# Optimization experiments

Hardware: AMD Instinct MI355X
Metric: run time of the kernel (lower is better)

Reference implementation:

```python
import jax, jax.numpy as jnp
import numpy as np

N, E, D, H = 100000, 1000000, 64, 64  # nodes, edges, input_dim, output_dim
EPS = 1e-5


def _lin(k, fi, fo):
    return jax.random.normal(k, (fi, fo), jnp.float32) / np.sqrt(fi)


def setup_inputs() -> dict:
    key = jax.random.key(0)
    ks = jax.random.split(key, 8)
    x = jax.random.normal(ks[0], (N, D), jnp.float32)
    e = jax.random.uniform(ks[1], (E,), jnp.float32)
    edge_index = jax.random.randint(ks[2], (2, E), 0, N, dtype=jnp.int32)
    return {
        "x": x,
        "e": e,
        "edge_index": edge_index,
        "W1": _lin(ks[3], 2 * D, H), "b1": jnp.zeros((H,), jnp.float32),
        "g1": jnp.ones((H,), jnp.float32), "be1": jnp.zeros((H,), jnp.float32),
        "W2": _lin(ks[4], H, H), "b2": jnp.zeros((H,), jnp.float32),
        "g2": jnp.ones((H,), jnp.float32), "be2": jnp.zeros((H,), jnp.float32),
        "W3": _lin(ks[5], H, H), "b3": jnp.zeros((H,), jnp.float32),
    }


def _layer_norm(h, g, b):
    mu = jnp.mean(h, axis=-1, keepdims=True)
    var = jnp.mean(jnp.square(h - mu), axis=-1, keepdims=True)
    return (h - mu) * jax.lax.rsqrt(var + EPS) * g + b


def reference(x, e, edge_index, W1, b1, g1, be1, W2, b2, g2, be2, W3, b3):
    start, end = edge_index[0], edge_index[1]
    we = e[:, None]  # [E,1]
    # edge-weighted gather-multiply-scatter_add, both directions
    mi = jax.ops.segment_sum(we * x[start], end, num_segments=N) \
       + jax.ops.segment_sum(we * x[end], start, num_segments=N)  # [N,D]
    h = jnp.concatenate([mi, x], axis=1)  # [N,2D]
    h = jnp.tanh(_layer_norm(h @ W1 + b1, g1, be1))
    h = jnp.tanh(_layer_norm(h @ W2 + b2, g2, be2))
    return h @ W3 + b3  # [N,H]
```

## Files before the change

### kernel.cpp

```cpp
#include <hip/hip_runtime.h>

typedef unsigned int u32;

#define NMAX 100000
#define EMAX 1000000
#define CAP 96
#define NSHMAX 12500

__device__ __align__(16) float g_mi[NMAX * 64];
__device__ int g_deg[8 * NSHMAX];
__device__ __align__(16) u32 g_adj[(size_t)8 * NSHMAX * CAP];

__global__ __launch_bounds__(256) void zero_deg(int n) {
    int i = blockIdx.x * 256 + threadIdx.x;
    if (i < n) g_deg[i] = 0;
}

__global__ __launch_bounds__(256) void fill_sharded(
    const int* __restrict__ src, const int* __restrict__ dst,
    const float* __restrict__ ew, int E, int NSH, int nchunk)
{
    int group = blockIdx.x & 7;
    int chunk = blockIdx.x >> 3;
    int stride = nchunk * 256;
    for (int e = chunk * 256 + threadIdx.x; e < E; e += stride) {
        int s = src[e], t = dst[e];
        float w = ew[e];
        int w15 = (int)(w * 32768.f + 0.5f);
        if (w15 > 32767) w15 = 32767;
        if ((s & 7) == group) {
            int idx = group * NSH + (s >> 3);
            int p = atomicAdd(&g_deg[idx], 1);
            if (p < CAP) g_adj[(size_t)idx * CAP + p] = ((u32)t << 15) | (u32)w15;
        }
        if ((t & 7) == group) {
            int idx = group * NSH + (t >> 3);
            int q = atomicAdd(&g_deg[idx], 1);
            if (q < CAP) g_adj[(size_t)idx * CAP + q] = ((u32)s << 15) | (u32)w15;
        }
    }
}

__global__ __launch_bounds__(256) void gather(const float* __restrict__ x,
                                              int N, int NSH) {
    int wid = (blockIdx.x * 256 + threadIdx.x) >> 6;
    int lane = threadIdx.x & 63;
    if (wid >= N) return;
    int idx = (wid & 7) * NSH + (wid >> 3);
    int cnt = g_deg[idx];
    if (cnt > CAP) cnt = CAP;
    const u32* row = g_adj + (size_t)idx * CAP;
    float acc = 0.f;

    for (int b = 0; b < cnt; b += 64) {
        int m = cnt - b;
        if (m > 64) m = 64;
        u32 ent = (lane < m) ? row[b + lane] : 0u;
        int nbr = (int)(ent >> 15);
        float wv = (float)(ent & 0x7FFFu) * (1.f / 32768.f);

        int j = 0;
        for (; j + 4 <= m; j += 4) {
            int n0 = __shfl(nbr, j + 0);
            int n1 = __shfl(nbr, j + 1);
            int n2 = __shfl(nbr, j + 2);
            int n3 = __shfl(nbr, j + 3);
            float w0 = __shfl(wv, j + 0);
            float w1 = __shfl(wv, j + 1);
            float w2 = __shfl(wv, j + 2);
            float w3 = __shfl(wv, j + 3);
            float v0 = x[(size_t)n0 * 64 + lane];
            float v1 = x[(size_t)n1 * 64 + lane];
            float v2 = x[(size_t)n2 * 64 + lane];
            float v3 = x[(size_t)n3 * 64 + lane];
            acc = fmaf(w0, v0, acc);
            acc = fmaf(w1, v1, acc);
            acc = fmaf(w2, v2, acc);
            acc = fmaf(w3, v3, acc);
        }
        for (; j < m; j++) {
            int nb = __shfl(nbr, j);
            float w = __shfl(wv, j);
            acc = fmaf(w, x[(size_t)nb * 64 + lane], acc);
        }
    }
    g_mi[(size_t)wid * 64 + lane] = acc;
}

#define MST 65

__global__ __launch_bounds__(128) void mlp(
    const float* __restrict__ x,
    const float* __restrict__ W1, const float* __restrict__ B1,
    const float* __restrict__ G1, const float* __restrict__ E1,
    const float* __restrict__ W2, const float* __restrict__ B2,
    const float* __restrict__ G2, const float* __restrict__ E2,
    const float* __restrict__ W3, const float* __restrict__ B3,
    float* __restrict__ out, int N)
{
    __shared__ float sb[128 * MST];

    int n0 = blockIdx.x * 128;
    int tid = threadIdx.x;
    int nodes = N - n0;
    if (nodes > 128) nodes = 128;
    bool act = tid < nodes;
    float h[64];

    for (int i = tid; i < 128 * 64; i += 128) {
        int nd = i >> 6, f = i & 63;
        if (nd < nodes) sb[nd * MST + f] = g_mi[(size_t)(n0 + nd) * 64 + f];
    }
    __syncthreads();
    if (act) {
        #pragma unroll
        for (int j = 0; j < 64; j++) h[j] = B1[j];
        for (int k = 0; k < 64; k++) {
            float a = sb[tid * MST + k];
            const float* wr = W1 + k * 64;
            #pragma unroll
            for (int j = 0; j < 64; j++) h[j] = fmaf(a, wr[j], h[j]);
        }
    }
    __syncthreads();

    for (int i = tid; i < 128 * 64; i += 128) {
        int nd = i >> 6, f = i & 63;
        if (nd < nodes) sb[nd * MST + f] = x[(size_t)(n0 + nd) * 64 + f];
    }
    __syncthreads();
    if (act) {
        for (int k = 0; k < 64; k++) {
            float a = sb[tid * MST + k];
            const float* wr = W1 + (64 + k) * 64;
            #pragma unroll
            for (int j = 0; j < 64; j++) h[j] = fmaf(a, wr[j], h[j]);
        }

        {
            float mu = 0.f;
            #pragma unroll
            for (int j = 0; j < 64; j++) mu += h[j];
            mu *= (1.f / 64.f);
            float var = 0.f;
            #pragma unroll
            for (int j = 0; j < 64; j++) { float d = h[j] - mu; var += d * d; }
            var *= (1.f / 64.f);
            float rs = rsqrtf(var + 1e-5f);
            #pragma unroll
            for (int j = 0; j < 64; j++) {
                float v = (h[j] - mu) * rs * G1[j] + E1[j];
                float ex = __expf(2.f * v);
                h[j] = 1.f - 2.f / (ex + 1.f);
            }
        }
        #pragma unroll
        for (int j = 0; j < 64; j++) sb[tid * MST + j] = h[j];

        #pragma unroll
        for (int j = 0; j < 64; j++) h[j] = B2[j];
        for (int k = 0; k < 64; k++) {
            float a = sb[tid * MST + k];
            const float* wr = W2 + k * 64;
            #pragma unroll
            for (int j = 0; j < 64; j++) h[j] = fmaf(a, wr[j], h[j]);
        }
        {
            float mu = 0.f;
            #pragma unroll
            for (int j = 0; j < 64; j++) mu += h[j];
            mu *= (1.f / 64.f);
            float var = 0.f;
            #pragma unroll
            for (int j = 0; j < 64; j++) { float d = h[j] - mu; var += d * d; }
            var *= (1.f / 64.f);
            float rs = rsqrtf(var + 1e-5f);
            #pragma unroll
            for (int j = 0; j < 64; j++) {
                float v = (h[j] - mu) * rs * G2[j] + E2[j];
                float ex = __expf(2.f * v);
                h[j] = 1.f - 2.f / (ex + 1.f);
            }
        }
        #pragma unroll
        for (int j = 0; j < 64; j++) sb[tid * MST + j] = h[j];

        #pragma unroll
        for (int j = 0; j < 64; j++) h[j] = B3[j];
        for (int k = 0; k < 64; k++) {
            float a = sb[tid * MST + k];
            const float* wr = W3 + k * 64;
            #pragma unroll
            for (int j = 0; j < 64; j++) h[j] = fmaf(a, wr[j], h[j]);
        }
        #pragma unroll
        for (int j = 0; j < 64; j++) sb[tid * MST + j] = h[j];
    }
    __syncthreads();

    for (int i = tid; i < 128 * 64; i += 128) {
        int nd = i >> 6, f = i & 63;
        if (nd < nodes) out[(size_t)(n0 + nd) * 64 + f] = sb[nd * MST + f];
    }
}

extern "C" void kernel_launch(void* const* d_in, const int* in_sizes, int n_in,
                              void* d_out, int out_size, void* d_ws, size_t ws_size,
                              hipStream_t stream) {
    const float* x  = (const float*)d_in[0];
    const float* e  = (const float*)d_in[1];
    const int* ei   = (const int*)d_in[2];
    const float* W1 = (const float*)d_in[3];
    const float* b1 = (const float*)d_in[4];
    const float* g1 = (const float*)d_in[5];
    const float* be1= (const float*)d_in[6];
    const float* W2 = (const float*)d_in[7];
    const float* b2 = (const float*)d_in[8];
    const float* g2 = (const float*)d_in[9];
    const float* be2= (const float*)d_in[10];
    const float* W3 = (const float*)d_in[11];
    const float* b3 = (const float*)d_in[12];

    int N = in_sizes[0] / 64;
    int E = in_sizes[1];
    int NSH = (N + 7) / 8;
    int ndeg = 8 * NSH;

    zero_deg<<<(ndeg + 255) / 256, 256, 0, stream>>>(ndeg);

    int nchunk = 256;
    fill_sharded<<<8 * nchunk, 256, 0, stream>>>(ei, ei + E, e, E, NSH, nchunk);

    gather<<<(N * 64 + 255) / 256, 256, 0, stream>>>(x, N, NSH);

    mlp<<<(N + 127) / 128, 128, 0, stream>>>(
        x, W1, b1, g1, be1, W2, b2, g2, be2, W3, b3, (float*)d_out, N);
}
```

Baseline: 380.7 us.

## Register-tile the fused MLP GEMMs with shared-memory weight chunks

Rewrites the per-node MLP kernel so that 256 threads compute each 128x64 layer output as 4x8 register tiles. Weights are staged through shared memory in 32-row chunks instead of each thread holding a 64-wide row and streaming uniform weight rows from global memory. The two halves of the first-layer input (mi and x) are loaded into one 129-stride buffer together. LayerNorm+tanh now runs on half the threads against shared memory. This trades more barriers and a larger LDS footprint, which may limit occupancy, for better FMA reuse. The float4 accesses on the odd 129 stride may also be misaligned.

```diff
diff --git a/kernel.cpp b/kernel.cpp
--- a/kernel.cpp
+++ b/kernel.cpp
@@ -87,9 +87,9 @@
     g_mi[(size_t)wid * 64 + lane] = acc;
 }
 
-#define MST 65
-
-__global__ __launch_bounds__(128) void mlp(
+#define HS 129
+
+__global__ __launch_bounds__(256) void mlp(
     const float* __restrict__ x,
     const float* __restrict__ W1, const float* __restrict__ B1,
     const float* __restrict__ G1, const float* __restrict__ E1,
@@ -98,109 +98,179 @@
     const float* __restrict__ W3, const float* __restrict__ B3,
     float* __restrict__ out, int N)
 {
-    __shared__ float sb[128 * MST];
-
+    __shared__ float hbuf[128 * HS];
+    __shared__ float Wc[32 * 64];
+    __shared__ float lnb[4 * 64];
+
+    int tid = threadIdx.x;
     int n0 = blockIdx.x * 128;
-    int tid = threadIdx.x;
-    int nodes = N - n0;
-    if (nodes > 128) nodes = 128;
-    bool act = tid < nodes;
-    float h[64];
-
-    for (int i = tid; i < 128 * 64; i += 128) {
+    int nodes = N - n0; if (nodes > 128) nodes = 128;
+
+    int tx = tid & 7;
+    int ty = tid >> 3;
+
+    if (tid < 64) {
+        lnb[tid]       = G1[tid];
+        lnb[64 + tid]  = E1[tid];
+        lnb[128 + tid] = G2[tid];
+        lnb[192 + tid] = E2[tid];
+    }
+
+    for (int i = tid; i < 128 * 64; i += 256) {
         int nd = i >> 6, f = i & 63;
-        if (nd < nodes) sb[nd * MST + f] = g_mi[(size_t)(n0 + nd) * 64 + f];
+        float vm = 0.f, vx = 0.f;
+        if (nd < nodes) {
+            size_t g = (size_t)(n0 + nd) * 64 + f;
+            vm = g_mi[g];
+            vx = x[g];
+        }
+        hbuf[nd * HS + f] = vm;
+        hbuf[nd * HS + 64 + f] = vx;
+    }
+
+    float acc[4][8];
+
+    {
+        float bc[8];
+        #pragma unroll
+        for (int c = 0; c < 8; c++) bc[c] = B1[tx * 8 + c];
+        #pragma unroll
+        for (int r = 0; r < 4; r++)
+            #pragma unroll
+            for (int c = 0; c < 8; c++) acc[r][c] = bc[c];
+
+        for (int kk = 0; kk < 128; kk += 32) {
+            __syncthreads();
+            for (int i = tid; i < 2048; i += 256)
+                Wc[i] = W1[(kk + (i >> 6)) * 64 + (i & 63)];
+            __syncthreads();
+            for (int k = 0; k < 32; k++) {
+                float4 w0 = *(const float4*)&Wc[k * 64 + tx * 8];
+                float4 w1 = *(const float4*)&Wc[k * 64 + tx * 8 + 4];
+                float w[8] = {w0.x, w0.y, w0.z, w0.w, w1.x, w1.y, w1.z, w1.w};
+                float a[4];
+                #pragma unroll
+                for (int r = 0; r < 4; r++) a[r] = hbuf[(ty * 4 + r) * HS + kk + k];
+                #pragma unroll
+                for (int r = 0; r < 4; r++)
+                    #pragma unroll
+                    for (int c = 0; c < 8; c++)
+                        acc[r][c] = fmaf(a[r], w[c], acc[r][c]);
+            }
+        }
     }
     __syncthreads();
-    if (act) {
-        #pragma unroll
-        for (int j = 0; j < 64; j++) h[j] = B1[j];
-        for (int k = 0; k < 64; k++) {
-            float a = sb[tid * MST + k];
-            const float* wr = W1 + k * 64;
+    #pragma unroll
+    for (int r = 0; r < 4; r++) {
+        *(float4*)&hbuf[(ty * 4 + r) * HS + tx * 8]     = make_float4(acc[r][0], acc[r][1], acc[r][2], acc[r][3]);
+        *(float4*)&hbuf[(ty * 4 + r) * HS + tx * 8 + 4] = make_float4(acc[r][4], acc[r][5], acc[r][6], acc[r][7]);
+    }
+    __syncthreads();
+
+    if (tid < 128) {
+        float mu = 0.f;
+        for (int j = 0; j < 64; j++) mu += hbuf[tid * HS + j];
+        mu *= (1.f / 64.f);
+        float var = 0.f;
+        for (int j = 0; j < 64; j++) { float d = hbuf[tid * HS + j] - mu; var += d * d; }
+        var *= (1.f / 64.f);
+        float rs = rsqrtf(var + 1e-5f);
+        for (int j = 0; j < 64; j++) {
+            float v = (hbuf[tid * HS + j] - mu) * rs * lnb[j] + lnb[64 + j];
+            float ex = __expf(2.f * v);
+            hbuf[tid * HS + j] = 1.f - 2.f / (ex + 1.f);
+        }
+    }
+
+    {
+        float bc[8];
+        #pragma unroll
+        for (int c = 0; c < 8; c++) bc[c] = B2[tx * 8 + c];
+        #pragma unroll
+        for (int r = 0; r < 4; r++)
             #pragma unroll
-            for (int j = 0; j < 64; j++) h[j] = fmaf(a, wr[j], h[j]);
+            for (int c = 0; c < 8; c++) acc[r][c] = bc[c];
+
+        for (int kk = 0; kk < 64; kk += 32) {
+            __syncthreads();
+            for (int i = tid; i < 2048; i += 256)
+                Wc[i] = W2[(kk + (i >> 6)) * 64 + (i & 63)];
+            __syncthreads();
+            for (int k = 0; k < 32; k++) {
+                float4 w0 = *(const float4*)&Wc[k * 64 + tx * 8];
+                float4 w1 = *(const float4*)&Wc[k * 64 + tx * 8 + 4];
+                float w[8] = {w0.x, w0.y, w0.z, w0.w, w1.x, w1.y, w1.z, w1.w};
+                float a[4];
+                #pragma unroll
+                for (int r = 0; r < 4; r++) a[r] = hbuf[(ty * 4 + r) * HS + kk + k];
+                #pragma unroll
+                for (int r = 0; r < 4; r++)
+                    #pragma unroll
+                    for (int c = 0; c < 8; c++)
+                        acc[r][c] = fmaf(a[r], w[c], acc[r][c]);
+            }
         }
     }
     __syncthreads();
-
-    for (int i = tid; i < 128 * 64; i += 128) {
-        int nd = i >> 6, f = i & 63;
-        if (nd < nodes) sb[nd * MST + f] = x[(size_t)(n0 + nd) * 64 + f];
+    #pragma unroll
+    for (int r = 0; r < 4; r++) {
+        *(float4*)&hbuf[(ty * 4 + r) * HS + tx * 8]     = make_float4(acc[r][0], acc[r][1], acc[r][2], acc[r][3]);
+        *(float4*)&hbuf[(ty * 4 + r) * HS + tx * 8 + 4] = make_float4(acc[r][4], acc[r][5], acc[r][6], acc[r][7]);
     }
     __syncthreads();
-    if (act) {
-        for (int k = 0; k < 64; k++) {
-            float a = sb[tid * MST + k];
-            const float* wr = W1 + (64 + k) * 64;
+
+    if (tid < 128) {
+        float mu = 0.f;
+        for (int j = 0; j < 64; j++) mu += hbuf[tid * HS + j];
+        mu *= (1.f / 64.f);
+        float var = 0.f;
+        for (int j = 0; j < 64; j++) { float d = hbuf[tid * HS + j] - mu; var += d * d; }
+        var *= (1.f / 64.f);
+        float rs = rsqrtf(var + 1e-5f);
+        for (int j = 0; j < 64; j++) {
+            float v = (hbuf[tid * HS + j] - mu) * rs * lnb[128 + j] + lnb[192 + j];
+            float ex = __expf(2.f * v);
+            hbuf[tid * HS + j] = 1.f - 2.f / (ex + 1.f);
+        }
+    }
+
+    {
+        float bc[8];
+        #pragma unroll
+        for (int c = 0; c < 8; c++) bc[c] = B3[tx * 8 + c];
+        #pragma unroll
+        for (int r = 0; r < 4; r++)
             #pragma unroll
-            for (int j = 0; j < 64; j++) h[j] = fmaf(a, wr[j], h[j]);
-        }
-
-        {
-            float mu = 0.f;
-            #pragma unroll
-            for (int j = 0; j < 64; j++) mu += h[j];
-            mu *= (1.f / 64.f);
-            float var = 0.f;
-            #pragma unroll
-            for (int j = 0; j < 64; j++) { float d = h[j] - mu; var += d * d; }
-            var *= (1.f / 64.f);
-            float rs = rsqrtf(var + 1e-5f);
-            #pragma unroll
-            for (int j = 0; j < 64; j++) {
-                float v = (h[j] - mu) * rs * G1[j] + E1[j];
-                float ex = __expf(2.f * v);
-                h[j] = 1.f - 2.f / (ex + 1.f);
+            for (int c = 0; c < 8; c++) acc[r][c] = bc[c];
+
+        for (int kk = 0; kk < 64; kk += 32) {
+            __syncthreads();
+            for (int i = tid; i < 2048; i += 256)
+                Wc[i] = W3[(kk + (i >> 6)) * 64 + (i & 63)];
+            __syncthreads();
+            for (int k = 0; k < 32; k++) {
+                float4 w0 = *(const float4*)&Wc[k * 64 + tx * 8];
+                float4 w1 = *(const float4*)&Wc[k * 64 + tx * 8 + 4];
+                float w[8] = {w0.x, w0.y, w0.z, w0.w, w1.x, w1.y, w1.z, w1.w};
+                float a[4];
+                #pragma unroll
+                for (int r = 0; r < 4; r++) a[r] = hbuf[(ty * 4 + r) * HS + kk + k];
+                #pragma unroll
+                for (int r = 0; r < 4; r++)
+                    #pragma unroll
+                    for (int c = 0; c < 8; c++)
+                        acc[r][c] = fmaf(a[r], w[c], acc[r][c]);
             }
         }
-        #pragma unroll
-        for (int j = 0; j < 64; j++) sb[tid * MST + j] = h[j];
-
-        #pragma unroll
-        for (int j = 0; j < 64; j++) h[j] = B2[j];
-        for (int k = 0; k < 64; k++) {
-            float a = sb[tid * MST + k];
-            const float* wr = W2 + k * 64;
-            #pragma unroll
-            for (int j = 0; j < 64; j++) h[j] = fmaf(a, wr[j], h[j]);
-        }
-        {
-            float mu = 0.f;
-            #pragma unroll
-            for (int j = 0; j < 64; j++) mu += h[j];
-            mu *= (1.f / 64.f);
-            float var = 0.f;
-            #pragma unroll
-            for (int j = 0; j < 64; j++) { float d = h[j] - mu; var += d * d; }
-            var *= (1.f / 64.f);
-            float rs = rsqrtf(var + 1e-5f);
-            #pragma unroll
-            for (int j = 0; j < 64; j++) {
-                float v = (h[j] - mu) * rs * G2[j] + E2[j];
-                float ex = __expf(2.f * v);
-                h[j] = 1.f - 2.f / (ex + 1.f);
-            }
-        }
-        #pragma unroll
-        for (int j = 0; j < 64; j++) sb[tid * MST + j] = h[j];
-
-        #pragma unroll
-        for (int j = 0; j < 64; j++) h[j] = B3[j];
-        for (int k = 0; k < 64; k++) {
-            float a = sb[tid * MST + k];
-            const float* wr = W3 + k * 64;
-            #pragma unroll
-            for (int j = 0; j < 64; j++) h[j] = fmaf(a, wr[j], h[j]);
-        }
-        #pragma unroll
-        for (int j = 0; j < 64; j++) sb[tid * MST + j] = h[j];
-    }
-    __syncthreads();
-
-    for (int i = tid; i < 128 * 64; i += 128) {
-        int nd = i >> 6, f = i & 63;
-        if (nd < nodes) out[(size_t)(n0 + nd) * 64 + f] = sb[nd * MST + f];
+    }
+    #pragma unroll
+    for (int r = 0; r < 4; r++) {
+        int nd = ty * 4 + r;
+        if (nd < nodes) {
+            float* po = out + (size_t)(n0 + nd) * 64 + tx * 8;
+            *(float4*)(po)     = make_float4(acc[r][0], acc[r][1], acc[r][2], acc[r][3]);
+            *(float4*)(po + 4) = make_float4(acc[r][4], acc[r][5], acc[r][6], acc[r][7]);
+        }
     }
 }
 
@@ -233,6 +303,6 @@
 
     gather<<<(N * 64 + 255) / 256, 256, 0, stream>>>(x, N, NSH);
 
-    mlp<<<(N + 127) / 128, 128, 0, stream>>>(
+    mlp<<<(N + 127) / 128, 256, 0, stream>>>(
         x, W1, b1, g1, be1, W2, b2, g2, be2, W3, b3, (float*)d_out, N);
 }
```

Measured after the change: 683.1 us. 1.79x slower.
